# Optimization experiments

Hardware: AMD Instinct MI355X
Metric: run time of the kernel (lower is better)

The kernel has to match this reference:

```python
import jax, jax.numpy as jnp
import numpy as np
import math

THETA = 10000.0

def apply_rope(x):
    # x: [B, H, S, D] with D even; interleaved even/odd rotation
    B, H, S, D = x.shape
    dim_half = D // 2
    freq_idx = jnp.arange(dim_half, dtype=jnp.float32)
    inv_freq = jnp.exp(-math.log(THETA) * freq_idx * 2.0 / D)  # [D/2]
    pos = jnp.arange(S, dtype=jnp.float32)
    angles = pos[:, None] * inv_freq[None, :]      # [S, D/2]
    cos = jnp.cos(angles)[None, None]              # [1,1,S,D/2]
    sin = jnp.sin(angles)[None, None]
    x_even = x[..., ::2]
    x_odd = x[..., 1::2]
    r_even = x_even * cos - x_odd * sin
    r_odd = x_odd * cos + x_even * sin
    return jnp.stack([r_even, r_odd], axis=-1).reshape(B, H, S, D)

def setup_inputs() -> dict:
    key = jax.random.key(0)
    ks = jax.random.split(key, 5)
    B, S, E = 2, 2048, 1024
    std = 0.02
    inp = {
        "hidden_states": jax.random.normal(ks[0], (B, S, E), dtype=jnp.float32),
        "Wq": jax.random.normal(ks[1], (E, E), dtype=jnp.float32) * std,
        "bq": jnp.zeros((E,), dtype=jnp.float32),
        "Wk": jax.random.normal(ks[2], (E, E), dtype=jnp.float32) * std,
        "bk": jnp.zeros((E,), dtype=jnp.float32),
        "Wv": jax.random.normal(ks[3], (E, E), dtype=jnp.float32) * std,
        "bv": jnp.zeros((E,), dtype=jnp.float32),
        "Wo": jax.random.normal(ks[4], (E, E), dtype=jnp.float32) * std,
        "bo": jnp.zeros((E,), dtype=jnp.float32),
    }
    return inp

def reference(hidden_states, Wq, bq, Wk, bk, Wv, bv, Wo, bo):
    NUM_HEADS = 16
    B, S, E = hidden_states.shape
    D = E // NUM_HEADS
    scale = 1.0 / math.sqrt(D)

    def proj(W, b):
        # torch Linear: x @ W.T + b; then [B,S,H,D] -> [B,H,S,D]
        y = hidden_states @ W.T + b
        return y.reshape(B, S, NUM_HEADS, D).transpose(0, 2, 1, 3)

    q = apply_rope(proj(Wq, bq))
    k = apply_rope(proj(Wk, bk))
    v = proj(Wv, bv)

    scores = jnp.einsum("bhqd,bhkd->bhqk", q, k) * scale
    attn = jax.nn.softmax(scores, axis=-1)
    out = jnp.einsum("bhqk,bhkd->bhqd", attn, v)  # [B,H,S,D]
    out = out.transpose(0, 2, 1, 3).reshape(B, S, E)
    return out @ Wo.T + bo  # dropout: eval mode (identity)
```

## Files before the change

### kernel.cpp

```cpp
#include <hip/hip_runtime.h>
#include <math.h>

#define B_ 2
#define S_ 2048
#define E_ 1024
#define H_ 16
#define D_ 64
#define M_ (B_*S_)
#define PT 32

typedef short bf16x8 __attribute__((ext_vector_type(8)));
typedef float f32x4 __attribute__((ext_vector_type(4)));
typedef unsigned short u16x4 __attribute__((ext_vector_type(4)));

__device__ __forceinline__ unsigned short f2bf(float f) {
    unsigned int u = __builtin_bit_cast(unsigned int, f);
    u += 0x7FFFu + ((u >> 16) & 1u);
    return (unsigned short)(u >> 16);
}
__device__ __forceinline__ f32x4 mfma16(bf16x8 a, bf16x8 b, f32x4 c) {
    return __builtin_amdgcn_mfma_f32_16x16x32_bf16(a, b, c, 0, 0, 0);
}
__device__ __forceinline__ bf16x8 cvt8(const float* p) {
    f32x4 lo = *(const f32x4*)p;
    f32x4 hi = *(const f32x4*)(p + 4);
    bf16x8 r;
#pragma unroll
    for (int e = 0; e < 4; e++) { r[e] = (short)f2bf(lo[e]); r[e + 4] = (short)f2bf(hi[e]); }
    return r;
}

__global__ __launch_bounds__(256, 3) void qkv_rope_kernel(
    const float* __restrict__ X,
    const float* __restrict__ Wq, const float* __restrict__ Wk,
    const float* __restrict__ Wv,
    const float* __restrict__ bq, const float* __restrict__ bk,
    const float* __restrict__ bv,
    unsigned short* __restrict__ Qo, unsigned short* __restrict__ Ko,
    unsigned short* __restrict__ Vo)
{
    __shared__ __align__(16) unsigned char lds_raw[128 * 132 * 2];
    unsigned short* As = (unsigned short*)lds_raw;
    unsigned short* Bs = (unsigned short*)(lds_raw + 128 * PT * 2);
    unsigned short* Cs = (unsigned short*)lds_raw;

    const int t = threadIdx.x;
    const int w = t >> 6, lane = t & 63, quad = lane >> 4, l16 = lane & 15;
    const int wr = (w >> 1) * 64, wc = (w & 1) * 64;
    const int n0 = blockIdx.x * 128, m0 = blockIdx.y * 128;
    const int z = blockIdx.z;
    const float* W    = (z == 0) ? Wq : (z == 1) ? Wk : Wv;
    const float* bias = (z == 0) ? bq : (z == 1) ? bk : bv;

    const int r4 = t >> 2, c8 = (t & 3) * 8;
    const int st = r4 * PT + c8;
    const float* Ag = X + (size_t)(m0 + r4) * E_ + c8;
    const float* Bg = W + (size_t)(n0 + r4) * E_ + c8;

    f32x4 zero = {0.f, 0.f, 0.f, 0.f};
    f32x4 acc[4][4];
#pragma unroll
    for (int i = 0; i < 4; i++)
#pragma unroll
        for (int j = 0; j < 4; j++) acc[i][j] = zero;

    for (int kt = 0; kt < E_; kt += 32) {
        bf16x8 a0 = cvt8(Ag + kt);
        bf16x8 a1 = cvt8(Ag + 64 * E_ + kt);
        bf16x8 b0 = cvt8(Bg + kt);
        bf16x8 b1 = cvt8(Bg + 64 * E_ + kt);
        __syncthreads();
        *(bf16x8*)&As[st]           = a0;
        *(bf16x8*)&As[st + 64 * PT] = a1;
        *(bf16x8*)&Bs[st]           = b0;
        *(bf16x8*)&Bs[st + 64 * PT] = b1;
        __syncthreads();
        bf16x8 af[4], bfr[4];
#pragma unroll
        for (int i = 0; i < 4; i++)
            af[i] = *(const bf16x8*)&As[(wr + i * 16 + l16) * PT + quad * 8];
#pragma unroll
        for (int j = 0; j < 4; j++)
            bfr[j] = *(const bf16x8*)&Bs[(wc + j * 16 + l16) * PT + quad * 8];
#pragma unroll
        for (int i = 0; i < 4; i++)
#pragma unroll
            for (int j = 0; j < 4; j++)
                acc[i][j] = mfma16(af[i], bfr[j], acc[i][j]);
    }

    __syncthreads();
    const int seg = quad;
    if (z < 2) {
        const float C = -0.41524101186091903f;
        const float INV2PI = 0.15915494309189535f;
#pragma unroll
        for (int j = 0; j < 4; j++) {
            int n_local = wc + j * 16 + l16;
            int n = n0 + n_local;
            int d = n & 63, f = d >> 1;
            float inv_rev = exp2f(C * (float)f) * INV2PI;
            float bvv = bias[n];
            float sgn = (d & 1) ? 1.f : -1.f;
#pragma unroll
            for (int i = 0; i < 4; i++) {
                int mb = wr + i * 16 + quad * 4;
#pragma unroll
                for (int r = 0; r < 4; r++) {
                    int m = m0 + mb + r;
                    int s = m & (S_ - 1);
                    float val = acc[i][j][r] + bvv;
                    float oth = __shfl_xor(val, 1);
                    float rev = (float)s * inv_rev;
                    float fr = rev - rintf(rev);
                    float sn = __builtin_amdgcn_sinf(fr);
                    float cs = __builtin_amdgcn_cosf(fr);
                    Cs[(mb + r) * 132 + n_local] = f2bf(val * cs + sgn * oth * sn);
                }
            }
        }
        __syncthreads();
        unsigned short* Out = (z == 0) ? Qo : Ko;
        const int btok = m0 >> 11;
        const int half = seg & 1;
#pragma unroll
        for (int it = 0; it < 16; it++) {
            int m_local = it * 8 + w * 2 + (seg >> 1);
            int s = (m0 + m_local) & (S_ - 1);
            int h = (n0 + half * 64) >> 6;
            u16x4 v = *(const u16x4*)&Cs[m_local * 132 + half * 64 + l16 * 4];
            *(u16x4*)&Out[(((size_t)btok * H_ + h) * S_ + s) * D_ + l16 * 4] = v;
        }
    } else {
#pragma unroll
        for (int j = 0; j < 4; j++) {
            int n_local = wc + j * 16 + l16;
            float bvv = bias[n0 + n_local];
#pragma unroll
            for (int i = 0; i < 4; i++) {
                int mb = wr + i * 16 + quad * 4;
#pragma unroll
                for (int r = 0; r < 4; r++)
                    Cs[n_local * 132 + mb + r] = f2bf(acc[i][j][r] + bvv);
            }
        }
        __syncthreads();
        const int btok = m0 >> 11;
        const int s0 = m0 & (S_ - 1);
        const int half = seg & 1;
#pragma unroll
        for (int it = 0; it < 16; it++) {
            int n_local = it * 8 + w * 2 + (seg >> 1);
            int n = n0 + n_local;
            int h = n >> 6, d = n & 63;
            u16x4 v = *(const u16x4*)&Cs[n_local * 132 + half * 64 + l16 * 4];
            *(u16x4*)&Vo[(((size_t)btok * H_ + h) * D_ + d) * S_ + s0 + half * 64 + l16 * 4] = v;
        }
    }
}

__global__ __launch_bounds__(512, 4) void attn_kernel(
    const unsigned short* __restrict__ Q, const unsigned short* __restrict__ K,
    const unsigned short* __restrict__ Vt, unsigned short* __restrict__ ctx)
{
    __shared__ unsigned short Ks[2][64 * 32];
    __shared__ unsigned short Vs[2][64 * 32];
    __shared__ unsigned short Ps[8][16 * 72];
    const int t = threadIdx.x;
    const int w = t >> 6, lane = t & 63, quad = lane >> 4, l16 = lane & 15;
    const int bh = blockIdx.y;
    const int q0 = blockIdx.x * 128 + w * 16;

    const unsigned short* Qg = Q + ((size_t)bh * S_ + q0) * D_;
    bf16x8 qf[2];
#pragma unroll
    for (int ks = 0; ks < 2; ks++)
        qf[ks] = *(const bf16x8*)(Qg + (size_t)l16 * 64 + ks * 32 + quad * 8);

    bf16x8 ones;
#pragma unroll
    for (int e = 0; e < 8; e++) ones[e] = (short)0x3F80;

    f32x4 zero = {0.f, 0.f, 0.f, 0.f};
    f32x4 acc_o[4];
    f32x4 acc_l = zero;
#pragma unroll
    for (int j = 0; j < 4; j++) acc_o[j] = zero;

    const int r8 = t >> 3;
    const int c8 = (t & 7) * 8;
    const int stKV = (c8 >> 5) * 2048 + r8 * 32 + (c8 & 31);
    unsigned short* KsF = &Ks[0][0];
    unsigned short* VsF = &Vs[0][0];
    const unsigned short* Kg0 = K + (size_t)bh * S_ * D_;
    const unsigned short* Vg0 = Vt + (size_t)bh * D_ * S_;

    const float SCL = 0.18033688011f;

    for (int kt = 0; kt < S_; kt += 64) {
        bf16x8 k0 = *(const bf16x8*)(Kg0 + (size_t)(kt + r8) * 64 + c8);
        bf16x8 v0 = *(const bf16x8*)(Vg0 + (size_t)r8 * S_ + kt + c8);
        __syncthreads();
        *(bf16x8*)&KsF[stKV] = k0;
        *(bf16x8*)&VsF[stKV] = v0;
        __syncthreads();

        f32x4 sc[4];
#pragma unroll
        for (int j = 0; j < 4; j++) sc[j] = zero;
#pragma unroll
        for (int ks = 0; ks < 2; ks++) {
#pragma unroll
            for (int j = 0; j < 4; j++) {
                bf16x8 kf = *(const bf16x8*)&Ks[ks][(j * 16 + l16) * 32 + quad * 8];
                sc[j] = mfma16(qf[ks], kf, sc[j]);
            }
        }
#pragma unroll
        for (int j = 0; j < 4; j++)
#pragma unroll
            for (int r = 0; r < 4; r++) {
                float p = __builtin_amdgcn_exp2f(sc[j][r] * SCL);
                Ps[w][(quad * 4 + r) * 72 + j * 16 + l16] = f2bf(p);
            }
#pragma unroll
        for (int ks = 0; ks < 2; ks++) {
            bf16x8 pf = *(const bf16x8*)&Ps[w][l16 * 72 + ks * 32 + quad * 8];
#pragma unroll
            for (int jd = 0; jd < 4; jd++) {
                bf16x8 vf = *(const bf16x8*)&Vs[ks][(jd * 16 + l16) * 32 + quad * 8];
                acc_o[jd] = mfma16(pf, vf, acc_o[jd]);
            }
            acc_l = mfma16(pf, ones, acc_l);
        }
    }

    const int b = bh >> 4, h = bh & 15;
    f32x4 rl;
#pragma unroll
    for (int r = 0; r < 4; r++) rl[r] = 1.0f / acc_l[r];
#pragma unroll
    for (int jd = 0; jd < 4; jd++)
#pragma unroll
        for (int r = 0; r < 4; r++) {
            int qrow = q0 + quad * 4 + r;
            int col = h * 64 + jd * 16 + l16;
            ctx[((size_t)b * S_ + qrow) * E_ + col] = f2bf(acc_o[jd][r] * rl[r]);
        }
}

__global__ __launch_bounds__(256, 2) void out_kernel(
    const unsigned short* __restrict__ Cx, const float* __restrict__ Wo,
    const float* __restrict__ bo, float* __restrict__ out)
{
    __shared__ unsigned short As[128 * PT];
    __shared__ unsigned short Bs[64 * PT];
    const int t = threadIdx.x;
    const int w = t >> 6, lane = t & 63, quad = lane >> 4, l16 = lane & 15;
    const int m0 = blockIdx.y * 128, n0 = blockIdx.x * 64;
    const int wr = w * 32;
    const int r4 = t >> 2, c8 = (t & 3) * 8;
    const int st = r4 * PT + c8;
    const unsigned short* Ag = Cx + (size_t)(m0 + r4) * E_ + c8;
    const float*          Bg = Wo + (size_t)(n0 + (r4 & 63)) * E_ + c8;

    f32x4 zero = {0.f, 0.f, 0.f, 0.f};
    f32x4 acc[2][4];
#pragma unroll
    for (int i = 0; i < 2; i++)
#pragma unroll
        for (int j = 0; j < 4; j++) acc[i][j] = zero;

    for (int kt = 0; kt < E_; kt += 32) {
        bf16x8 a0 = *(const bf16x8*)(Ag + kt);
        bf16x8 a1 = *(const bf16x8*)(Ag + 64 * E_ + kt);
        bf16x8 b0 = cvt8(Bg + kt);
        __syncthreads();
        *(bf16x8*)&As[st]           = a0;
        *(bf16x8*)&As[st + 64 * PT] = a1;
        *(bf16x8*)&Bs[st]           = b0;
        __syncthreads();
        bf16x8 af[2], bfr[4];
#pragma unroll
        for (int i = 0; i < 2; i++)
            af[i] = *(const bf16x8*)&As[(wr + i * 16 + l16) * PT + quad * 8];
#pragma unroll
        for (int j = 0; j < 4; j++)
            bfr[j] = *(const bf16x8*)&Bs[(j * 16 + l16) * PT + quad * 8];
#pragma unroll
        for (int i = 0; i < 2; i++)
#pragma unroll
            for (int j = 0; j < 4; j++)
                acc[i][j] = mfma16(af[i], bfr[j], acc[i][j]);
    }

#pragma unroll
    for (int j = 0; j < 4; j++) {
        int n = n0 + j * 16 + l16;
        float bvv = bo[n];
#pragma unroll
        for (int i = 0; i < 2; i++) {
            int mrow = m0 + wr + i * 16 + quad * 4;
#pragma unroll
            for (int r = 0; r < 4; r++)
                out[(size_t)(mrow + r) * E_ + n] = acc[i][j][r] + bvv;
        }
    }
}

extern "C" void kernel_launch(void* const* d_in, const int* in_sizes, int n_in,
                              void* d_out, int out_size, void* d_ws, size_t ws_size,
                              hipStream_t stream) {
    const float* X  = (const float*)d_in[0];
    const float* Wq = (const float*)d_in[1];
    const float* bq = (const float*)d_in[2];
    const float* Wk = (const float*)d_in[3];
    const float* bk = (const float*)d_in[4];
    const float* Wv = (const float*)d_in[5];
    const float* bv = (const float*)d_in[6];
    const float* Wo = (const float*)d_in[7];
    const float* bo = (const float*)d_in[8];
    float* outp = (float*)d_out;

    const size_t TN = (size_t)B_ * H_ * S_ * D_;
    if (ws_size < 4 * TN * sizeof(unsigned short)) return;

    unsigned short* Qb = (unsigned short*)d_ws;
    unsigned short* Kb = Qb + TN;
    unsigned short* Vb = Kb + TN;
    unsigned short* Cx = Vb + TN;

    qkv_rope_kernel<<<dim3(E_ / 128, M_ / 128, 3), 256, 0, stream>>>(
        X, Wq, Wk, Wv, bq, bk, bv, Qb, Kb, Vb);
    attn_kernel<<<dim3(S_ / 128, B_ * H_), 512, 0, stream>>>(Qb, Kb, Vb, Cx);
    out_kernel<<<dim3(E_ / 64, M_ / 128), 256, 0, stream>>>(Cx, Wo, bo, outp);
}
```

Measured before the change: 218.9 us.

## Pre-convert inputs to bf16 and stage tiles via direct global-to-LDS loads

Adds a conversion kernel that casts X and all four weight matrices to bf16 once per call. The QKV and output GEMMs then read bf16 and fill LDS with global_load_lds, with no register staging or per-tile conversion. The attention kernel's K/V tile loads also switch to direct global-to-LDS transfers, with an unpadded LDS layout. This removes repeated fp32 loads and conversions in the GEMM loops, at the cost of an extra kernel launch and an extra pass over the inputs. It also risks LDS bank conflicts from the unpadded layout. The old fp32 path is kept as a fallback when the workspace is too small.

```diff
diff --git a/kernel.cpp b/kernel.cpp
--- a/kernel.cpp
+++ b/kernel.cpp
@@ -29,11 +29,29 @@
     for (int e = 0; e < 4; e++) { r[e] = (short)f2bf(lo[e]); r[e + 4] = (short)f2bf(hi[e]); }
     return r;
 }
-
-__global__ __launch_bounds__(256, 3) void qkv_rope_kernel(
-    const float* __restrict__ X,
-    const float* __restrict__ Wq, const float* __restrict__ Wk,
-    const float* __restrict__ Wv,
+__device__ __forceinline__ void g2l16(const unsigned short* g, unsigned short* l) {
+    __builtin_amdgcn_global_load_lds(
+        (const __attribute__((address_space(1))) unsigned int*)(const void*)g,
+        (__attribute__((address_space(3))) unsigned int*)(void*)l,
+        16, 0, 0);
+}
+
+__global__ __launch_bounds__(256) void cvt_kernel(
+    const float* __restrict__ X,  const float* __restrict__ Wq,
+    const float* __restrict__ Wk, const float* __restrict__ Wv,
+    const float* __restrict__ Wo,
+    unsigned short* __restrict__ Xb, unsigned short* __restrict__ Wb)
+{
+    const int y = blockIdx.y;
+    const float* src = (y == 0) ? X : (y == 1) ? Wq : (y == 2) ? Wk : (y == 3) ? Wv : Wo;
+    unsigned short* dst = (y == 0) ? Xb : Wb + (size_t)(y - 1) * (E_ * E_);
+    const size_t n = (y == 0) ? (size_t)M_ * E_ : (size_t)E_ * E_;
+    size_t i = ((size_t)blockIdx.x * 256 + threadIdx.x) * 8;
+    if (i < n) *(bf16x8*)(dst + i) = cvt8(src + i);
+}
+
+__global__ __launch_bounds__(256, 4) void qkv_rope_bf(
+    const unsigned short* __restrict__ Xb, const unsigned short* __restrict__ Wb,
     const float* __restrict__ bq, const float* __restrict__ bk,
     const float* __restrict__ bv,
     unsigned short* __restrict__ Qo, unsigned short* __restrict__ Ko,
@@ -41,7 +59,7 @@
 {
     __shared__ __align__(16) unsigned char lds_raw[128 * 132 * 2];
     unsigned short* As = (unsigned short*)lds_raw;
-    unsigned short* Bs = (unsigned short*)(lds_raw + 128 * PT * 2);
+    unsigned short* Bs = (unsigned short*)(lds_raw + 8192);
     unsigned short* Cs = (unsigned short*)lds_raw;
 
     const int t = threadIdx.x;
@@ -49,13 +67,12 @@
     const int wr = (w >> 1) * 64, wc = (w & 1) * 64;
     const int n0 = blockIdx.x * 128, m0 = blockIdx.y * 128;
     const int z = blockIdx.z;
-    const float* W    = (z == 0) ? Wq : (z == 1) ? Wk : Wv;
+    const unsigned short* W = Wb + (size_t)z * (E_ * E_);
     const float* bias = (z == 0) ? bq : (z == 1) ? bk : bv;
 
     const int r4 = t >> 2, c8 = (t & 3) * 8;
-    const int st = r4 * PT + c8;
-    const float* Ag = X + (size_t)(m0 + r4) * E_ + c8;
-    const float* Bg = W + (size_t)(n0 + r4) * E_ + c8;
+    const unsigned short* Ag = Xb + (size_t)(m0 + r4) * E_ + c8;
+    const unsigned short* Bg = W  + (size_t)(n0 + r4) * E_ + c8;
 
     f32x4 zero = {0.f, 0.f, 0.f, 0.f};
     f32x4 acc[4][4];
@@ -65,23 +82,19 @@
         for (int j = 0; j < 4; j++) acc[i][j] = zero;
 
     for (int kt = 0; kt < E_; kt += 32) {
-        bf16x8 a0 = cvt8(Ag + kt);
-        bf16x8 a1 = cvt8(Ag + 64 * E_ + kt);
-        bf16x8 b0 = cvt8(Bg + kt);
-        bf16x8 b1 = cvt8(Bg + 64 * E_ + kt);
-        __syncthreads();
-        *(bf16x8*)&As[st]           = a0;
-        *(bf16x8*)&As[st + 64 * PT] = a1;
-        *(bf16x8*)&Bs[st]           = b0;
-        *(bf16x8*)&Bs[st + 64 * PT] = b1;
+        __syncthreads();
+        g2l16(Ag + kt,           &As[t * 8]);
+        g2l16(Ag + 64 * E_ + kt, &As[t * 8 + 2048]);
+        g2l16(Bg + kt,           &Bs[t * 8]);
+        g2l16(Bg + 64 * E_ + kt, &Bs[t * 8 + 2048]);
         __syncthreads();
         bf16x8 af[4], bfr[4];
 #pragma unroll
         for (int i = 0; i < 4; i++)
-            af[i] = *(const bf16x8*)&As[(wr + i * 16 + l16) * PT + quad * 8];
+            af[i] = *(const bf16x8*)&As[(wr + i * 16 + l16) * 32 + quad * 8];
 #pragma unroll
         for (int j = 0; j < 4; j++)
-            bfr[j] = *(const bf16x8*)&Bs[(wc + j * 16 + l16) * PT + quad * 8];
+            bfr[j] = *(const bf16x8*)&Bs[(wc + j * 16 + l16) * 32 + quad * 8];
 #pragma unroll
         for (int i = 0; i < 4; i++)
 #pragma unroll
@@ -187,40 +200,37 @@
 #pragma unroll
     for (int j = 0; j < 4; j++) acc_o[j] = zero;
 
-    const int r8 = t >> 3;
-    const int c8 = (t & 7) * 8;
-    const int stKV = (c8 >> 5) * 2048 + r8 * 32 + (c8 & 31);
+    const int tt = t & 255, ksel = t >> 8;
+    const int sr = tt >> 2, sc = (tt & 3) * 8;
     unsigned short* KsF = &Ks[0][0];
     unsigned short* VsF = &Vs[0][0];
-    const unsigned short* Kg0 = K + (size_t)bh * S_ * D_;
-    const unsigned short* Vg0 = Vt + (size_t)bh * D_ * S_;
+    const unsigned short* Kg0 = K  + (size_t)bh * S_ * D_ + (size_t)sr * 64 + ksel * 32 + sc;
+    const unsigned short* Vg0 = Vt + (size_t)bh * D_ * S_ + (size_t)sr * S_ + ksel * 32 + sc;
 
     const float SCL = 0.18033688011f;
 
     for (int kt = 0; kt < S_; kt += 64) {
-        bf16x8 k0 = *(const bf16x8*)(Kg0 + (size_t)(kt + r8) * 64 + c8);
-        bf16x8 v0 = *(const bf16x8*)(Vg0 + (size_t)r8 * S_ + kt + c8);
-        __syncthreads();
-        *(bf16x8*)&KsF[stKV] = k0;
-        *(bf16x8*)&VsF[stKV] = v0;
-        __syncthreads();
-
-        f32x4 sc[4];
-#pragma unroll
-        for (int j = 0; j < 4; j++) sc[j] = zero;
+        __syncthreads();
+        g2l16(Kg0 + (size_t)kt * 64, &KsF[t * 8]);
+        g2l16(Vg0 + kt,              &VsF[t * 8]);
+        __syncthreads();
+
+        f32x4 sc4[4];
+#pragma unroll
+        for (int j = 0; j < 4; j++) sc4[j] = zero;
 #pragma unroll
         for (int ks = 0; ks < 2; ks++) {
 #pragma unroll
             for (int j = 0; j < 4; j++) {
                 bf16x8 kf = *(const bf16x8*)&Ks[ks][(j * 16 + l16) * 32 + quad * 8];
-                sc[j] = mfma16(qf[ks], kf, sc[j]);
+                sc4[j] = mfma16(qf[ks], kf, sc4[j]);
             }
         }
 #pragma unroll
         for (int j = 0; j < 4; j++)
 #pragma unroll
             for (int r = 0; r < 4; r++) {
-                float p = __builtin_amdgcn_exp2f(sc[j][r] * SCL);
+                float p = __builtin_amdgcn_exp2f(sc4[j][r] * SCL);
                 Ps[w][(quad * 4 + r) * 72 + j * 16 + l16] = f2bf(p);
             }
 #pragma unroll
@@ -249,7 +259,191 @@
         }
 }
 
-__global__ __launch_bounds__(256, 2) void out_kernel(
+__global__ __launch_bounds__(256, 4) void out_bf(
+    const unsigned short* __restrict__ Cx, const unsigned short* __restrict__ Wob,
+    const float* __restrict__ bo, float* __restrict__ out)
+{
+    __shared__ unsigned short As[128 * 32];
+    __shared__ unsigned short Bs[64 * 32];
+    const int t = threadIdx.x;
+    const int w = t >> 6, lane = t & 63, quad = lane >> 4, l16 = lane & 15;
+    const int m0 = blockIdx.y * 128, n0 = blockIdx.x * 64;
+    const int wr = w * 32;
+    const int r4 = t >> 2, c8 = (t & 3) * 8;
+    const unsigned short* Ag = Cx  + (size_t)(m0 + r4) * E_ + c8;
+    const unsigned short* Bg = Wob + (size_t)(n0 + r4) * E_ + c8;
+
+    f32x4 zero = {0.f, 0.f, 0.f, 0.f};
+    f32x4 acc[2][4];
+#pragma unroll
+    for (int i = 0; i < 2; i++)
+#pragma unroll
+        for (int j = 0; j < 4; j++) acc[i][j] = zero;
+
+    for (int kt = 0; kt < E_; kt += 32) {
+        __syncthreads();
+        g2l16(Ag + kt,           &As[t * 8]);
+        g2l16(Ag + 64 * E_ + kt, &As[t * 8 + 2048]);
+        g2l16(Bg + kt,           &Bs[t * 8]);
+        __syncthreads();
+        bf16x8 af[2], bfr[4];
+#pragma unroll
+        for (int i = 0; i < 2; i++)
+            af[i] = *(const bf16x8*)&As[(wr + i * 16 + l16) * 32 + quad * 8];
+#pragma unroll
+        for (int j = 0; j < 4; j++)
+            bfr[j] = *(const bf16x8*)&Bs[(j * 16 + l16) * 32 + quad * 8];
+#pragma unroll
+        for (int i = 0; i < 2; i++)
+#pragma unroll
+            for (int j = 0; j < 4; j++)
+                acc[i][j] = mfma16(af[i], bfr[j], acc[i][j]);
+    }
+
+#pragma unroll
+    for (int j = 0; j < 4; j++) {
+        int n = n0 + j * 16 + l16;
+        float bvv = bo[n];
+#pragma unroll
+        for (int i = 0; i < 2; i++) {
+            int mrow = m0 + wr + i * 16 + quad * 4;
+#pragma unroll
+            for (int r = 0; r < 4; r++)
+                out[(size_t)(mrow + r) * E_ + n] = acc[i][j][r] + bvv;
+        }
+    }
+}
+
+__global__ __launch_bounds__(256, 3) void qkv_rope_f32(
+    const float* __restrict__ X,
+    const float* __restrict__ Wq, const float* __restrict__ Wk,
+    const float* __restrict__ Wv,
+    const float* __restrict__ bq, const float* __restrict__ bk,
+    const float* __restrict__ bv,
+    unsigned short* __restrict__ Qo, unsigned short* __restrict__ Ko,
+    unsigned short* __restrict__ Vo)
+{
+    __shared__ __align__(16) unsigned char lds_raw[128 * 132 * 2];
+    unsigned short* As = (unsigned short*)lds_raw;
+    unsigned short* Bs = (unsigned short*)(lds_raw + 8192);
+    unsigned short* Cs = (unsigned short*)lds_raw;
+
+    const int t = threadIdx.x;
+    const int w = t >> 6, lane = t & 63, quad = lane >> 4, l16 = lane & 15;
+    const int wr = (w >> 1) * 64, wc = (w & 1) * 64;
+    const int n0 = blockIdx.x * 128, m0 = blockIdx.y * 128;
+    const int z = blockIdx.z;
+    const float* W    = (z == 0) ? Wq : (z == 1) ? Wk : Wv;
+    const float* bias = (z == 0) ? bq : (z == 1) ? bk : bv;
+
+    const int r4 = t >> 2, c8 = (t & 3) * 8;
+    const int st = r4 * PT + c8;
+    const float* Ag = X + (size_t)(m0 + r4) * E_ + c8;
+    const float* Bg = W + (size_t)(n0 + r4) * E_ + c8;
+
+    f32x4 zero = {0.f, 0.f, 0.f, 0.f};
+    f32x4 acc[4][4];
+#pragma unroll
+    for (int i = 0; i < 4; i++)
+#pragma unroll
+        for (int j = 0; j < 4; j++) acc[i][j] = zero;
+
+    for (int kt = 0; kt < E_; kt += 32) {
+        bf16x8 a0 = cvt8(Ag + kt);
+        bf16x8 a1 = cvt8(Ag + 64 * E_ + kt);
+        bf16x8 b0 = cvt8(Bg + kt);
+        bf16x8 b1 = cvt8(Bg + 64 * E_ + kt);
+        __syncthreads();
+        *(bf16x8*)&As[st]           = a0;
+        *(bf16x8*)&As[st + 64 * PT] = a1;
+        *(bf16x8*)&Bs[st]           = b0;
+        *(bf16x8*)&Bs[st + 64 * PT] = b1;
+        __syncthreads();
+        bf16x8 af[4], bfr[4];
+#pragma unroll
+        for (int i = 0; i < 4; i++)
+            af[i] = *(const bf16x8*)&As[(wr + i * 16 + l16) * PT + quad * 8];
+#pragma unroll
+        for (int j = 0; j < 4; j++)
+            bfr[j] = *(const bf16x8*)&Bs[(wc + j * 16 + l16) * PT + quad * 8];
+#pragma unroll
+        for (int i = 0; i < 4; i++)
+#pragma unroll
+            for (int j = 0; j < 4; j++)
+                acc[i][j] = mfma16(af[i], bfr[j], acc[i][j]);
+    }
+
+    __syncthreads();
+    const int seg = quad;
+    if (z < 2) {
+        const float C = -0.41524101186091903f;
+        const float INV2PI = 0.15915494309189535f;
+#pragma unroll
+        for (int j = 0; j < 4; j++) {
+            int n_local = wc + j * 16 + l16;
+            int n = n0 + n_local;
+            int d = n & 63, f = d >> 1;
+            float inv_rev = exp2f(C * (float)f) * INV2PI;
+            float bvv = bias[n];
+            float sgn = (d & 1) ? 1.f : -1.f;
+#pragma unroll
+            for (int i = 0; i < 4; i++) {
+                int mb = wr + i * 16 + quad * 4;
+#pragma unroll
+                for (int r = 0; r < 4; r++) {
+                    int m = m0 + mb + r;
+                    int s = m & (S_ - 1);
+                    float val = acc[i][j][r] + bvv;
+                    float oth = __shfl_xor(val, 1);
+                    float rev = (float)s * inv_rev;
+                    float fr = rev - rintf(rev);
+                    float sn = __builtin_amdgcn_sinf(fr);
+                    float cs = __builtin_amdgcn_cosf(fr);
+                    Cs[(mb + r) * 132 + n_local] = f2bf(val * cs + sgn * oth * sn);
+                }
+            }
+        }
+        __syncthreads();
+        unsigned short* Out = (z == 0) ? Qo : Ko;
+        const int btok = m0 >> 11;
+        const int half = seg & 1;
+#pragma unroll
+        for (int it = 0; it < 16; it++) {
+            int m_local = it * 8 + w * 2 + (seg >> 1);
+            int s = (m0 + m_local) & (S_ - 1);
+            int h = (n0 + half * 64) >> 6;
+            u16x4 v = *(const u16x4*)&Cs[m_local * 132 + half * 64 + l16 * 4];
+            *(u16x4*)&Out[(((size_t)btok * H_ + h) * S_ + s) * D_ + l16 * 4] = v;
+        }
+    } else {
+#pragma unroll
+        for (int j = 0; j < 4; j++) {
+            int n_local = wc + j * 16 + l16;
+            float bvv = bias[n0 + n_local];
+#pragma unroll
+            for (int i = 0; i < 4; i++) {
+                int mb = wr + i * 16 + quad * 4;
+#pragma unroll
+                for (int r = 0; r < 4; r++)
+                    Cs[n_local * 132 + mb + r] = f2bf(acc[i][j][r] + bvv);
+            }
+        }
+        __syncthreads();
+        const int btok = m0 >> 11;
+        const int s0 = m0 & (S_ - 1);
+        const int half = seg & 1;
+#pragma unroll
+        for (int it = 0; it < 16; it++) {
+            int n_local = it * 8 + w * 2 + (seg >> 1);
+            int n = n0 + n_local;
+            int h = n >> 6, d = n & 63;
+            u16x4 v = *(const u16x4*)&Cs[n_local * 132 + half * 64 + l16 * 4];
+            *(u16x4*)&Vo[(((size_t)btok * H_ + h) * D_ + d) * S_ + s0 + half * 64 + l16 * 4] = v;
+        }
+    }
+}
+
+__global__ __launch_bounds__(256, 2) void out_f32(
     const unsigned short* __restrict__ Cx, const float* __restrict__ Wo,
     const float* __restrict__ bo, float* __restrict__ out)
 {
@@ -328,10 +522,23 @@
     unsigned short* Qb = (unsigned short*)d_ws;
     unsigned short* Kb = Qb + TN;
     unsigned short* Vb = Kb + TN;
-    unsigned short* Cx = Vb + TN;
-
-    qkv_rope_kernel<<<dim3(E_ / 128, M_ / 128, 3), 256, 0, stream>>>(
-        X, Wq, Wk, Wv, bq, bk, bv, Qb, Kb, Vb);
-    attn_kernel<<<dim3(S_ / 128, B_ * H_), 512, 0, stream>>>(Qb, Kb, Vb, Cx);
-    out_kernel<<<dim3(E_ / 64, M_ / 128), 256, 0, stream>>>(Cx, Wo, bo, outp);
-}
+
+    if (ws_size >= 5 * TN * sizeof(unsigned short)) {
+        unsigned short* Xb = Vb + TN;
+        unsigned short* Wb = Xb + TN;
+        unsigned short* Cx = Xb;
+
+        cvt_kernel<<<dim3(2048, 5), 256, 0, stream>>>(X, Wq, Wk, Wv, Wo, Xb, Wb);
+        qkv_rope_bf<<<dim3(E_ / 128, M_ / 128, 3), 256, 0, stream>>>(
+            Xb, Wb, bq, bk, bv, Qb, Kb, Vb);
+        attn_kernel<<<dim3(S_ / 128, B_ * H_), 512, 0, stream>>>(Qb, Kb, Vb, Cx);
+        out_bf<<<dim3(E_ / 64, M_ / 128), 256, 0, stream>>>(
+            Cx, Wb + 3 * (size_t)(E_ * E_), bo, outp);
+    } else {
+        unsigned short* Cx = Vb + TN;
+        qkv_rope_f32<<<dim3(E_ / 128, M_ / 128, 3), 256, 0, stream>>>(
+            X, Wq, Wk, Wv, bq, bk, bv, Qb, Kb, Vb);
+        attn_kernel<<<dim3(S_ / 128, B_ * H_), 512, 0, stream>>>(Qb, Kb, Vb, Cx);
+        out_f32<<<dim3(E_ / 64, M_ / 128), 256, 0, stream>>>(Cx, Wo, bo, outp);
+    }
+}
```

Measured after the change: 208.1 us. 4.9% less time.
